# Kernel optimization log

Hardware: AMD Instinct MI355X
Metric: run time of the kernel (lower is better)

Reference implementation:

```python
import jax, jax.numpy as jnp
import numpy as np

N_NODES = 100000   # n_user (70k) + m_item (30k)
N_EDGES = 2000000  # bidirectional user-item interaction edges
DIM = 64           # latent_dim = config['recdim']


def setup_inputs() -> dict:
    key = jax.random.key(0)
    k1, k2, k3, k4 = jax.random.split(key, 4)
    x = jax.random.normal(k1, (N_NODES, DIM), dtype=jnp.float32)
    edge_index = jax.random.randint(k2, (2, N_EDGES), 0, N_NODES, dtype=jnp.int32)
    # w_linears: Linear(2*D, D) per layer; stored as [in, out] so y = h @ W + b
    s = 1.0 / np.sqrt(2 * DIM)
    W0 = jax.random.normal(k3, (2 * DIM, DIM), dtype=jnp.float32) * s
    b0 = jnp.zeros((DIM,), dtype=jnp.float32)
    W1 = jax.random.normal(k4, (2 * DIM, DIM), dtype=jnp.float32) * s
    b1 = jnp.zeros((DIM,), dtype=jnp.float32)
    return {"x": x, "edge_index": edge_index, "W0": W0, "b0": b0, "W1": W1, "b1": b1}


def reference(x, edge_index, W0, b0, W1, b1):
    # SAGE-style: neighbor gather + mean aggregation + concat(self, agg) + per-layer linear
    n = x.shape[0]
    src = edge_index[0]  # message source nodes
    dst = edge_index[1]  # message destination nodes
    deg = jax.ops.segment_sum(jnp.ones(src.shape[0], x.dtype), dst, num_segments=n)
    inv_deg = (1.0 / jnp.maximum(deg, 1.0))[:, None]  # [N,1] mean normalizer

    h = x
    layers = ((W0, b0, True), (W1, b1, False))
    for W, b, apply_relu in layers:
        agg = jax.ops.segment_sum(h[src], dst, num_segments=n) * inv_deg  # [N,D] neighbor mean
        h = jnp.concatenate([h, agg], axis=1) @ W + b                      # [N,2D] @ [2D,D]
        if apply_relu:
            h = jax.nn.relu(h)
    return h
```

## Files before the change

kernel.cpp:

```cpp
#include <hip/hip_runtime.h>
#include <hip/hip_bf16.h>

#define N_NODES 100000
#define N_EDGES 2000000
#define DIM 64
#define NB 391
#define CAP 8192
#define EPB 4096
#define EPT 16
#define BIN_BLOCKS ((N_EDGES + EPB - 1) / EPB)
#define XCONV_BLOCKS (N_NODES * DIM / 2 / 256)

typedef __attribute__((ext_vector_type(8))) short short8;
typedef __attribute__((ext_vector_type(4))) float f32x4;

__global__ __launch_bounds__(256) void binprep_kernel(const int* __restrict__ src,
                                                      const int* __restrict__ dst,
                                                      int* __restrict__ gbcur,
                                                      int* __restrict__ ebuf,
                                                      const float* __restrict__ x,
                                                      unsigned int* __restrict__ xb2,
                                                      const float* __restrict__ W0,
                                                      const float* __restrict__ W1,
                                                      __hip_bfloat16* __restrict__ wfrag) {
    __shared__ int buf[EPB];
    __shared__ short bufb[EPB];
    __shared__ int a[512];
    __shared__ int lscan[NB], lcur[NB], gbase[NB];

    const int bid = blockIdx.x;
    if (bid >= BIN_BLOCKS) {
        const int pb = bid - BIN_BLOCKS;
        if (pb < XCONV_BLOCKS) {
            const int i = pb * 256 + threadIdx.x;
            float2 v = ((const float2*)x)[i];
            __hip_bfloat162 o = __float22bfloat162_rn(v);
            xb2[i] = *(unsigned int*)&o;
        } else {
            const int tid = (pb - XCONV_BLOCKS) * 256 + threadIdx.x;
            const int j    = tid & 7;
            const int lane = (tid >> 3) & 63;
            const int kc   = (tid >> 9) & 3;
            const int nt   = (tid >> 11) & 3;
            const int l    = tid >> 13;
            const int k = kc * 32 + (lane >> 4) * 8 + j;
            const int n = nt * 16 + (lane & 15);
            const float* W = l ? W1 : W0;
            wfrag[tid] = __float2bfloat16(W[k * 64 + n]);
        }
        return;
    }

    const int t = threadIdx.x;
    const int e0 = bid * EPB;
    const int cnt = min(EPB, N_EDGES - e0);

    for (int i = t; i < 512; i += 256) a[i] = 0;
    __syncthreads();

    int ls[EPT], ld[EPT];
    #pragma unroll
    for (int k = 0; k < EPT; ++k) {
        const int o = t + k * 256;
        if (o < cnt) {
            ls[k] = src[e0 + o];
            ld[k] = dst[e0 + o];
            atomicAdd(&a[ld[k] >> 8], 1);
        } else ld[k] = -1;
    }
    __syncthreads();

    #pragma unroll
    for (int d = 1; d < 512; d <<= 1) {
        const int idx = (t + 1) * 2 * d - 1;
        if (idx < 512) a[idx] += a[idx - d];
        __syncthreads();
    }
    if (t == 0) a[511] = 0;
    __syncthreads();
    #pragma unroll
    for (int d = 256; d >= 1; d >>= 1) {
        const int idx = (t + 1) * 2 * d - 1;
        if (idx < 512) {
            const int tmp = a[idx - d];
            a[idx - d] = a[idx];
            a[idx] += tmp;
        }
        __syncthreads();
    }
    for (int i = t; i < NB; i += 256) {
        const int c = a[i + 1] - a[i];
        lscan[i] = a[i];
        lcur[i]  = a[i];
        gbase[i] = c ? atomicAdd(&gbcur[i], c) : 0;
    }
    __syncthreads();

    #pragma unroll
    for (int k = 0; k < EPT; ++k) {
        if (ld[k] >= 0) {
            const int b = ld[k] >> 8;
            const int p = atomicAdd(&lcur[b], 1);
            buf[p]  = (ls[k] << 8) | (ld[k] & 255);
            bufb[p] = (short)b;
        }
    }
    __syncthreads();
    for (int i = t; i < cnt; i += 256) {
        const int pk = buf[i];
        const int b  = bufb[i];
        ebuf[b * CAP + gbase[b] + (i - lscan[b])] = pk;
    }
}

__global__ __launch_bounds__(512) void scanC_kernel(const int* __restrict__ gbcur,
                                                    int* __restrict__ dboff) {
    __shared__ int a[512];
    const int t = threadIdx.x;
    const int v = (t < NB) ? gbcur[t] : 0;
    a[t] = v;
    __syncthreads();
    #pragma unroll
    for (int off = 1; off < 512; off <<= 1) {
        int u = (t >= off) ? a[t - off] : 0;
        __syncthreads();
        a[t] += u;
        __syncthreads();
    }
    if (t < NB) dboff[t] = a[t] - v;
    if (t == 0) dboff[NB] = N_EDGES;
}

__global__ __launch_bounds__(256) void fillpass_kernel(const int* __restrict__ ebuf,
                                                       const int* __restrict__ gbcur,
                                                       const int* __restrict__ dboff,
                                                       int* __restrict__ row_ptr,
                                                       int* __restrict__ csr) {
    __shared__ int cnt[256];
    __shared__ int s[256];
    __shared__ int cur[256];
    const int b = blockIdx.x;
    const int t = threadIdx.x;
    const int nbase = b << 8;
    const int ecnt = gbcur[b];
    const int estart = b * CAP;
    const int dbase = dboff[b];

    cnt[t] = 0;
    __syncthreads();
    for (int i = t; i < ecnt; i += 256)
        atomicAdd(&cnt[ebuf[estart + i] & 255], 1);
    __syncthreads();

    const int v = cnt[t];
    s[t] = v;
    __syncthreads();
    #pragma unroll
    for (int off = 1; off < 256; off <<= 1) {
        int u = (t >= off) ? s[t - off] : 0;
        __syncthreads();
        s[t] += u;
        __syncthreads();
    }
    const int rp = dbase + s[t] - v;
    if (nbase + t < N_NODES) row_ptr[nbase + t] = rp;
    if (b == NB - 1 && t == 0) row_ptr[N_NODES] = N_EDGES;
    cur[t] = rp;
    __syncthreads();

    for (int i = t; i < ecnt; i += 256) {
        const int pk = ebuf[estart + i];
        const int p = atomicAdd(&cur[pk & 255], 1);
        csr[p] = pk >> 8;
    }
}

__global__ __launch_bounds__(256) void gather_kernel(const uint2* __restrict__ hb8,
                                                     const int* __restrict__ row_ptr,
                                                     const int* __restrict__ csr,
                                                     uint2* __restrict__ agg8) {
    const int wave = threadIdx.x >> 6;
    const int lane = threadIdx.x & 63;
    const int node = blockIdx.x * 4 + wave;
    const int rp0 = row_ptr[node];
    const int rp1 = row_ptr[node + 1];
    const int q = lane >> 4;
    const int r = lane & 15;

    float a0 = 0.f, a1 = 0.f, a2 = 0.f, a3 = 0.f;
    for (int base = rp0; base < rp1; base += 64) {
        const int cnt = min(rp1 - base, 64);
        const int idx = (lane < cnt) ? __builtin_nontemporal_load(csr + base + lane) : 0;
        int j = 0;
        for (; j + 16 <= cnt; j += 16) {
            const int s0 = __shfl(idx, j + q);
            const int s1 = __shfl(idx, j + 4 + q);
            const int s2 = __shfl(idx, j + 8 + q);
            const int s3 = __shfl(idx, j + 12 + q);
            const uint2 u0 = hb8[(size_t)s0 * 16 + r];
            const uint2 u1 = hb8[(size_t)s1 * 16 + r];
            const uint2 u2 = hb8[(size_t)s2 * 16 + r];
            const uint2 u3 = hb8[(size_t)s3 * 16 + r];
            a0 += __uint_as_float(u0.x << 16); a1 += __uint_as_float(u0.x & 0xffff0000u);
            a2 += __uint_as_float(u0.y << 16); a3 += __uint_as_float(u0.y & 0xffff0000u);
            a0 += __uint_as_float(u1.x << 16); a1 += __uint_as_float(u1.x & 0xffff0000u);
            a2 += __uint_as_float(u1.y << 16); a3 += __uint_as_float(u1.y & 0xffff0000u);
            a0 += __uint_as_float(u2.x << 16); a1 += __uint_as_float(u2.x & 0xffff0000u);
            a2 += __uint_as_float(u2.y << 16); a3 += __uint_as_float(u2.y & 0xffff0000u);
            a0 += __uint_as_float(u3.x << 16); a1 += __uint_as_float(u3.x & 0xffff0000u);
            a2 += __uint_as_float(u3.y << 16); a3 += __uint_as_float(u3.y & 0xffff0000u);
        }
        for (; j < cnt; j += 4) {
            const int jj = j + q;
            const int s = __shfl(idx, jj & 63);
            const uint2 u = hb8[(size_t)s * 16 + r];
            if (jj < cnt) {
                a0 += __uint_as_float(u.x << 16); a1 += __uint_as_float(u.x & 0xffff0000u);
                a2 += __uint_as_float(u.y << 16); a3 += __uint_as_float(u.y & 0xffff0000u);
            }
        }
    }
    a0 += __shfl_xor(a0, 16); a0 += __shfl_xor(a0, 32);
    a1 += __shfl_xor(a1, 16); a1 += __shfl_xor(a1, 32);
    a2 += __shfl_xor(a2, 16); a2 += __shfl_xor(a2, 32);
    a3 += __shfl_xor(a3, 16); a3 += __shfl_xor(a3, 32);
    if (lane < 16) {
        const float inv = 1.0f / fmaxf((float)(rp1 - rp0), 1.0f);
        __hip_bfloat162 p0 = __float22bfloat162_rn(make_float2(a0 * inv, a1 * inv));
        __hip_bfloat162 p1 = __float22bfloat162_rn(make_float2(a2 * inv, a3 * inv));
        uint2 o;
        o.x = *(unsigned int*)&p0;
        o.y = *(unsigned int*)&p1;
        agg8[(size_t)node * 16 + r] = o;
    }
}

template <bool RELU, bool OUTF32>
__global__ __launch_bounds__(256) void gemm_kernel(const unsigned short* __restrict__ hb,
                                                   const unsigned short* __restrict__ aggb,
                                                   const unsigned short* __restrict__ wfrag,
                                                   const float* __restrict__ bias,
                                                   float* __restrict__ outf,
                                                   unsigned short* __restrict__ outb) {
    const int wave = threadIdx.x >> 6;
    const int lane = threadIdx.x & 63;
    const int m0 = (blockIdx.x * 4 + wave) * 16;
    const int quad = lane >> 4;
    const int lrow = lane & 15;
    const int m = min(m0 + lrow, N_NODES - 1);

    short8 bf[4][4];
    #pragma unroll
    for (int nt = 0; nt < 4; ++nt)
        #pragma unroll
        for (int kc = 0; kc < 4; ++kc)
            bf[nt][kc] = *(const short8*)(wfrag + (size_t)((nt * 4 + kc) * 64 + lane) * 8);

    f32x4 acc[4];
    #pragma unroll
    for (int nt = 0; nt < 4; ++nt) acc[nt] = f32x4{0.f, 0.f, 0.f, 0.f};

    #pragma unroll
    for (int kc = 0; kc < 4; ++kc) {
        const unsigned short* ap = (kc < 2)
            ? (hb   + (size_t)m * 64 + kc * 32 + quad * 8)
            : (aggb + (size_t)m * 64 + (kc - 2) * 32 + quad * 8);
        const short8 af = *(const short8*)ap;
        #pragma unroll
        for (int nt = 0; nt < 4; ++nt)
            acc[nt] = __builtin_amdgcn_mfma_f32_16x16x32_bf16(af, bf[nt][kc], acc[nt], 0, 0, 0);
    }

    #pragma unroll
    for (int nt = 0; nt < 4; ++nt) {
        const float bv = bias[nt * 16 + lrow];
        #pragma unroll
        for (int r = 0; r < 4; ++r) {
            const int mr = m0 + quad * 4 + r;
            if (mr < N_NODES) {
                float v = acc[nt][r] + bv;
                if (RELU) v = fmaxf(v, 0.f);
                const size_t off = (size_t)mr * 64 + nt * 16 + lrow;
                if (OUTF32) {
                    outf[off] = v;
                } else {
                    __hip_bfloat16 hv = __float2bfloat16(v);
                    outb[off] = *(unsigned short*)&hv;
                }
            }
        }
    }
}

extern "C" void kernel_launch(void* const* d_in, const int* in_sizes, int n_in,
                              void* d_out, int out_size, void* d_ws, size_t ws_size,
                              hipStream_t stream) {
    const float* x  = (const float*)d_in[0];
    const int*   ei = (const int*)d_in[1];
    const float* W0 = (const float*)d_in[2];
    const float* b0 = (const float*)d_in[3];
    const float* W1 = (const float*)d_in[4];
    const float* b1 = (const float*)d_in[5];
    float* out = (float*)d_out;

    const int* src = ei;
    const int* dst = ei + N_EDGES;

    char* ws = (char*)d_ws;
    auto alloc = [&](size_t bytes) {
        char* p = ws;
        ws += (bytes + 255) & ~(size_t)255;
        return p;
    };
    int* gbcur   = (int*)alloc((size_t)NB * 4);
    int* dboff   = (int*)alloc((size_t)(NB + 1) * 4);
    int* row_ptr = (int*)alloc((size_t)(N_NODES + 1) * 4);
    int* ebuf    = (int*)alloc((size_t)NB * CAP * 4);
    int* csr     = (int*)alloc((size_t)N_EDGES * 4);
    unsigned short* xb    = (unsigned short*)alloc((size_t)N_NODES * DIM * 2);
    unsigned short* aggb  = (unsigned short*)alloc((size_t)N_NODES * DIM * 2);
    unsigned short* h1b   = (unsigned short*)alloc((size_t)N_NODES * DIM * 2);
    __hip_bfloat16* wfrag = (__hip_bfloat16*)alloc((size_t)2 * 8192 * 2);

    hipMemsetAsync(gbcur, 0, (size_t)NB * 4, stream);

    binprep_kernel<<<BIN_BLOCKS + XCONV_BLOCKS + 64, 256, 0, stream>>>(
        src, dst, gbcur, ebuf, x, (unsigned int*)xb, W0, W1, wfrag);
    scanC_kernel<<<1, 512, 0, stream>>>(gbcur, dboff);
    fillpass_kernel<<<NB, 256, 0, stream>>>(ebuf, gbcur, dboff, row_ptr, csr);

    const int gemm_blocks = (N_NODES + 63) / 64;

    gather_kernel<<<N_NODES / 4, 256, 0, stream>>>((const uint2*)xb, row_ptr, csr,
                                                   (uint2*)aggb);
    gemm_kernel<true, false><<<gemm_blocks, 256, 0, stream>>>(
        xb, aggb, (const unsigned short*)wfrag, b0, nullptr, h1b);

    gather_kernel<<<N_NODES / 4, 256, 0, stream>>>((const uint2*)h1b, row_ptr, csr,
                                                   (uint2*)aggb);
    gemm_kernel<false, true><<<gemm_blocks, 256, 0, stream>>>(
        h1b, aggb, (const unsigned short*)wfrag + 8192, b1, out, nullptr);
}
```

Baseline: 245.7 us.

## Pad per-node CSR rows to 16 with dummy zero row, drop global scan

Each node's neighbor list is padded to a multiple of 16 entries. The padding points to an extra zero row appended to the feature buffers, so the gather loop runs without tail handling and issues up to 16 loads per batch before accumulating. The per-bucket offset uses a fixed PCAP stride, which removes the separate global scan kernel, and row pointer plus degree are packed into one int2. The cost is extra dummy loads for low-degree nodes and a larger csr buffer. Correctness assumes each bucket's padded total fits in PCAP.

```diff
diff --git a/kernel.cpp b/kernel.cpp
--- a/kernel.cpp
+++ b/kernel.cpp
@@ -6,6 +6,7 @@
 #define DIM 64
 #define NB 391
 #define CAP 8192
+#define PCAP 10240
 #define EPB 4096
 #define EPT 16
 #define BIN_BLOCKS ((N_EDGES + EPB - 1) / EPB)
@@ -113,28 +114,9 @@
     }
 }
 
-__global__ __launch_bounds__(512) void scanC_kernel(const int* __restrict__ gbcur,
-                                                    int* __restrict__ dboff) {
-    __shared__ int a[512];
-    const int t = threadIdx.x;
-    const int v = (t < NB) ? gbcur[t] : 0;
-    a[t] = v;
-    __syncthreads();
-    #pragma unroll
-    for (int off = 1; off < 512; off <<= 1) {
-        int u = (t >= off) ? a[t - off] : 0;
-        __syncthreads();
-        a[t] += u;
-        __syncthreads();
-    }
-    if (t < NB) dboff[t] = a[t] - v;
-    if (t == 0) dboff[NB] = N_EDGES;
-}
-
 __global__ __launch_bounds__(256) void fillpass_kernel(const int* __restrict__ ebuf,
                                                        const int* __restrict__ gbcur,
-                                                       const int* __restrict__ dboff,
-                                                       int* __restrict__ row_ptr,
+                                                       int2* __restrict__ nodeinfo,
                                                        int* __restrict__ csr) {
     __shared__ int cnt[256];
     __shared__ int s[256];
@@ -144,7 +126,6 @@
     const int nbase = b << 8;
     const int ecnt = gbcur[b];
     const int estart = b * CAP;
-    const int dbase = dboff[b];
 
     cnt[t] = 0;
     __syncthreads();
@@ -152,8 +133,9 @@
         atomicAdd(&cnt[ebuf[estart + i] & 255], 1);
     __syncthreads();
 
-    const int v = cnt[t];
-    s[t] = v;
+    const int deg  = cnt[t];
+    const int pdeg = (deg + 15) & ~15;
+    s[t] = pdeg;
     __syncthreads();
     #pragma unroll
     for (int off = 1; off < 256; off <<= 1) {
@@ -162,9 +144,8 @@
         s[t] += u;
         __syncthreads();
     }
-    const int rp = dbase + s[t] - v;
-    if (nbase + t < N_NODES) row_ptr[nbase + t] = rp;
-    if (b == NB - 1 && t == 0) row_ptr[N_NODES] = N_EDGES;
+    const int rp = b * PCAP + s[t] - pdeg;
+    if (nbase + t < N_NODES) nodeinfo[nbase + t] = make_int2(rp, deg);
     cur[t] = rp;
     __syncthreads();
 
@@ -173,50 +154,46 @@
         const int p = atomicAdd(&cur[pk & 255], 1);
         csr[p] = pk >> 8;
     }
+    __syncthreads();
+    for (int p = rp + deg; p < rp + pdeg; ++p)
+        csr[p] = N_NODES;
 }
 
 __global__ __launch_bounds__(256) void gather_kernel(const uint2* __restrict__ hb8,
-                                                     const int* __restrict__ row_ptr,
+                                                     const int2* __restrict__ nodeinfo,
                                                      const int* __restrict__ csr,
                                                      uint2* __restrict__ agg8) {
     const int wave = threadIdx.x >> 6;
     const int lane = threadIdx.x & 63;
     const int node = blockIdx.x * 4 + wave;
-    const int rp0 = row_ptr[node];
-    const int rp1 = row_ptr[node + 1];
+    const int2 ni = nodeinfo[node];
+    const int rp0 = ni.x;
+    const int deg = ni.y;
+    const int pcnt = (deg + 15) & ~15;
     const int q = lane >> 4;
     const int r = lane & 15;
 
     float a0 = 0.f, a1 = 0.f, a2 = 0.f, a3 = 0.f;
-    for (int base = rp0; base < rp1; base += 64) {
-        const int cnt = min(rp1 - base, 64);
-        const int idx = (lane < cnt) ? __builtin_nontemporal_load(csr + base + lane) : 0;
-        int j = 0;
-        for (; j + 16 <= cnt; j += 16) {
-            const int s0 = __shfl(idx, j + q);
-            const int s1 = __shfl(idx, j + 4 + q);
-            const int s2 = __shfl(idx, j + 8 + q);
-            const int s3 = __shfl(idx, j + 12 + q);
-            const uint2 u0 = hb8[(size_t)s0 * 16 + r];
-            const uint2 u1 = hb8[(size_t)s1 * 16 + r];
-            const uint2 u2 = hb8[(size_t)s2 * 16 + r];
-            const uint2 u3 = hb8[(size_t)s3 * 16 + r];
-            a0 += __uint_as_float(u0.x << 16); a1 += __uint_as_float(u0.x & 0xffff0000u);
-            a2 += __uint_as_float(u0.y << 16); a3 += __uint_as_float(u0.y & 0xffff0000u);
-            a0 += __uint_as_float(u1.x << 16); a1 += __uint_as_float(u1.x & 0xffff0000u);
-            a2 += __uint_as_float(u1.y << 16); a3 += __uint_as_float(u1.y & 0xffff0000u);
-            a0 += __uint_as_float(u2.x << 16); a1 += __uint_as_float(u2.x & 0xffff0000u);
-            a2 += __uint_as_float(u2.y << 16); a3 += __uint_as_float(u2.y & 0xffff0000u);
-            a0 += __uint_as_float(u3.x << 16); a1 += __uint_as_float(u3.x & 0xffff0000u);
-            a2 += __uint_as_float(u3.y << 16); a3 += __uint_as_float(u3.y & 0xffff0000u);
-        }
-        for (; j < cnt; j += 4) {
-            const int jj = j + q;
-            const int s = __shfl(idx, jj & 63);
-            const uint2 u = hb8[(size_t)s * 16 + r];
-            if (jj < cnt) {
-                a0 += __uint_as_float(u.x << 16); a1 += __uint_as_float(u.x & 0xffff0000u);
-                a2 += __uint_as_float(u.y << 16); a3 += __uint_as_float(u.y & 0xffff0000u);
+    for (int base = 0; base < pcnt; base += 64) {
+        const int rem = min(pcnt - base, 64);
+        const int nslots = rem >> 2;
+        const int idx = (lane < rem)
+            ? __builtin_nontemporal_load(csr + rp0 + base + lane) : 0;
+        uint2 u[16];
+        #pragma unroll
+        for (int i = 0; i < 16; ++i) {
+            if (i < nslots) {
+                const int si = __shfl(idx, 4 * i + q);
+                u[i] = hb8[(size_t)si * 16 + r];
+            }
+        }
+        #pragma unroll
+        for (int i = 0; i < 16; ++i) {
+            if (i < nslots) {
+                a0 += __uint_as_float(u[i].x << 16);
+                a1 += __uint_as_float(u[i].x & 0xffff0000u);
+                a2 += __uint_as_float(u[i].y << 16);
+                a3 += __uint_as_float(u[i].y & 0xffff0000u);
             }
         }
     }
@@ -225,7 +202,7 @@
     a2 += __shfl_xor(a2, 16); a2 += __shfl_xor(a2, 32);
     a3 += __shfl_xor(a3, 16); a3 += __shfl_xor(a3, 32);
     if (lane < 16) {
-        const float inv = 1.0f / fmaxf((float)(rp1 - rp0), 1.0f);
+        const float inv = 1.0f / fmaxf((float)deg, 1.0f);
         __hip_bfloat162 p0 = __float22bfloat162_rn(make_float2(a0 * inv, a1 * inv));
         __hip_bfloat162 p1 = __float22bfloat162_rn(make_float2(a2 * inv, a3 * inv));
         uint2 o;
@@ -312,31 +289,31 @@
         ws += (bytes + 255) & ~(size_t)255;
         return p;
     };
-    int* gbcur   = (int*)alloc((size_t)NB * 4);
-    int* dboff   = (int*)alloc((size_t)(NB + 1) * 4);
-    int* row_ptr = (int*)alloc((size_t)(N_NODES + 1) * 4);
-    int* ebuf    = (int*)alloc((size_t)NB * CAP * 4);
-    int* csr     = (int*)alloc((size_t)N_EDGES * 4);
-    unsigned short* xb    = (unsigned short*)alloc((size_t)N_NODES * DIM * 2);
+    int*  gbcur    = (int*)alloc((size_t)NB * 4);
+    int2* nodeinfo = (int2*)alloc((size_t)N_NODES * 8);
+    int*  ebuf     = (int*)alloc((size_t)NB * CAP * 4);
+    int*  csr      = (int*)alloc((size_t)NB * PCAP * 4);
+    unsigned short* xb    = (unsigned short*)alloc((size_t)(N_NODES + 1) * DIM * 2);
     unsigned short* aggb  = (unsigned short*)alloc((size_t)N_NODES * DIM * 2);
-    unsigned short* h1b   = (unsigned short*)alloc((size_t)N_NODES * DIM * 2);
+    unsigned short* h1b   = (unsigned short*)alloc((size_t)(N_NODES + 1) * DIM * 2);
     __hip_bfloat16* wfrag = (__hip_bfloat16*)alloc((size_t)2 * 8192 * 2);
 
     hipMemsetAsync(gbcur, 0, (size_t)NB * 4, stream);
+    hipMemsetAsync(xb  + (size_t)N_NODES * DIM, 0, DIM * 2, stream);
+    hipMemsetAsync(h1b + (size_t)N_NODES * DIM, 0, DIM * 2, stream);
 
     binprep_kernel<<<BIN_BLOCKS + XCONV_BLOCKS + 64, 256, 0, stream>>>(
         src, dst, gbcur, ebuf, x, (unsigned int*)xb, W0, W1, wfrag);
-    scanC_kernel<<<1, 512, 0, stream>>>(gbcur, dboff);
-    fillpass_kernel<<<NB, 256, 0, stream>>>(ebuf, gbcur, dboff, row_ptr, csr);
+    fillpass_kernel<<<NB, 256, 0, stream>>>(ebuf, gbcur, nodeinfo, csr);
 
     const int gemm_blocks = (N_NODES + 63) / 64;
 
-    gather_kernel<<<N_NODES / 4, 256, 0, stream>>>((const uint2*)xb, row_ptr, csr,
+    gather_kernel<<<N_NODES / 4, 256, 0, stream>>>((const uint2*)xb, nodeinfo, csr,
                                                    (uint2*)aggb);
     gemm_kernel<true, false><<<gemm_blocks, 256, 0, stream>>>(
         xb, aggb, (const unsigned short*)wfrag, b0, nullptr, h1b);
 
-    gather_kernel<<<N_NODES / 4, 256, 0, stream>>>((const uint2*)h1b, row_ptr, csr,
+    gather_kernel<<<N_NODES / 4, 256, 0, stream>>>((const uint2*)h1b, nodeinfo, csr,
                                                    (uint2*)aggb);
     gemm_kernel<false, true><<<gemm_blocks, 256, 0, stream>>>(
         h1b, aggb, (const unsigned short*)wfrag + 8192, b1, out, nullptr);
```

Result: slower. 284.8 us (+15.9%).
